# Performance work log

Measured on AMD Instinct MI355X. Metric: run time of the kernel, lower is better.

The kernel has to match this reference:

```python
import jax, jax.numpy as jnp
import numpy as np

TEMPERATURE = 0.1
PROTO_M = 0.999
EPS = 1e-12


def _l2norm(x, axis):
    return x / jnp.clip(jnp.linalg.norm(x, axis=axis, keepdims=True), EPS)


def setup_inputs() -> dict:
    key = jax.random.key(0)
    k1, k2, k3, k4, k5 = jax.random.split(key, 5)
    B, D, K, C = 1024, 128, 65536, 1000
    q = _l2norm(jax.random.normal(k1, (B, D), dtype=jnp.float32), axis=1)
    k = _l2norm(jax.random.normal(k2, (B, D), dtype=jnp.float32), axis=1)
    queue = _l2norm(jax.random.normal(k3, (D, K), dtype=jnp.float32), axis=0)
    prototypes = _l2norm(jax.random.normal(k4, (C, D), dtype=jnp.float32), axis=1)
    target = jax.random.randint(k5, (B,), 0, C, dtype=jnp.int64)
    return {"q": q, "k": k, "queue": queue, "prototypes": prototypes, "target": target}


def reference(q, k, queue, prototypes, target):
    B = q.shape[0]
    C = prototypes.shape[0]

    # contrastive logits: positive is q.k, negatives against the queue
    l_pos = jnp.einsum('nc,nc->n', q, k)[:, None]            # [B, 1]
    l_neg = jnp.einsum('nc,ck->nk', q, queue)                # [B, K]
    logits = jnp.concatenate([l_pos, l_neg], axis=1) / TEMPERATURE

    # prototypical logits
    logits_proto = jnp.einsum('nc,pc->np', q, prototypes) / TEMPERATURE  # [B, C]

    # dequeue/enqueue: ptr = 0 (single device, fresh queue_ptr)
    new_queue = jax.lax.dynamic_update_slice(queue, k.T, (0, 0))

    # sequential per-sample prototype EMA, vectorized in closed form:
    # if class c receives features f_1..f_m (in batch order), the final value is
    #   proto_c * m_p^m + (1 - m_p) * sum_j m_p^(m - j) * f_j
    onehot = jax.nn.one_hot(target, C, dtype=q.dtype)        # [B, C]
    cum = jnp.cumsum(onehot, axis=0)                         # inclusive per-class counts
    occ = jnp.take_along_axis(cum, target[:, None], axis=1)[:, 0]  # j for each sample
    n_c = cum[-1]                                            # [C] total hits per class
    w = (1.0 - PROTO_M) * PROTO_M ** (n_c[target] - occ)     # [B]
    acc = jax.ops.segment_sum(w[:, None] * q, target, num_segments=C)  # [C, D]
    new_prototypes = prototypes * (PROTO_M ** n_c)[:, None] + acc
    new_prototypes = _l2norm(new_prototypes, axis=1)

    return logits, logits_proto, new_queue, new_prototypes
```

## Files before the change

### kernel.cpp

```cpp
#include <hip/hip_runtime.h>
#include <hip/hip_bf16.h>

typedef __bf16 bf16x8 __attribute__((ext_vector_type(8)));
typedef float  f32x4  __attribute__((ext_vector_type(4)));


#define B_   1024
#define D_   128
#define K_   65536
#define C_   1000
#define LROW 65537
#define TINV 10.0f

__global__ __launch_bounds__(256) void prep(const float* __restrict__ queue,
                                            const float* __restrict__ q,
                                            const float* __restrict__ k,
                                            __bf16* __restrict__ Bt,
                                            __bf16* __restrict__ qbf,
                                            float* __restrict__ logits) {
    __shared__ __bf16 Lt[128 * 128];
    const int tid = threadIdx.x;

    if (blockIdx.x < 512) {
        char* ltb = (char*)Lt;
        const int c0 = blockIdx.x * 128;
        #pragma unroll
        for (int it = 0; it < 16; ++it) {
            const int idx = it * 256 + tid;
            const int d   = idx >> 5;
            const int cq  = (idx & 31) * 4;
            const f32x4 v = *reinterpret_cast<const f32x4*>(queue + (size_t)d * K_ + c0 + cq);
            const int db = d >> 3, de = (d & 7) * 2;
            #pragma unroll
            for (int jj = 0; jj < 4; ++jj) {
                const int c = cq + jj;
                *reinterpret_cast<__bf16*>(ltb + c * 256 + ((db ^ ((c >> 2) & 15)) << 4) + de)
                    = (__bf16)v[jj];
            }
        }
        __syncthreads();
        #pragma unroll
        for (int it = 0; it < 8; ++it) {
            const int idx = it * 256 + tid;
            const int c   = idx >> 4;
            const int db  = idx & 15;
            const bf16x8 v = *reinterpret_cast<const bf16x8*>(
                ltb + c * 256 + ((db ^ ((c >> 2) & 15)) << 4));
            *reinterpret_cast<bf16x8*>(Bt + (size_t)(c0 + c) * D_ + db * 8) = v;
        }
    } else {
        const int wid  = tid >> 6;
        const int lane = tid & 63;
        const int row  = (blockIdx.x - 512) * 4 + wid;
        const float2 qv = reinterpret_cast<const float2*>(q + (size_t)row * D_)[lane];
        const float2 kv = reinterpret_cast<const float2*>(k + (size_t)row * D_)[lane];
        union { __bf16 h[2]; unsigned int u; } u2;
        u2.h[0] = (__bf16)(qv.x * TINV);
        u2.h[1] = (__bf16)(qv.y * TINV);
        reinterpret_cast<unsigned int*>(qbf)[row * 64 + lane] = u2.u;
        float p = qv.x * kv.x + qv.y * kv.y;
        #pragma unroll
        for (int off = 32; off > 0; off >>= 1) p += __shfl_xor(p, off);
        if (lane == 0) logits[(size_t)row * LROW] = p * TINV;
    }
}

#define MG_QCOPY 512
#define MG_PROTO 1008
#define MG_PUPD  500
#define MG_PRE   (MG_QCOPY + MG_PROTO + MG_PUPD)
__global__ __launch_bounds__(256) void mega(const __bf16* __restrict__ qbf,
                                            const __bf16* __restrict__ Bt,
                                            const float* __restrict__ queue,
                                            const float* __restrict__ k,
                                            const float* __restrict__ q,
                                            const float* __restrict__ protos,
                                            const int* __restrict__ target,
                                            float* __restrict__ logits,
                                            float* __restrict__ lproto,
                                            float* __restrict__ outq,
                                            float* __restrict__ outp) {
    __shared__ char smem[16384];
    const int tid = threadIdx.x;
    const int bid = blockIdx.x;

    if (bid < MG_QCOPY) {
        const int d  = bid >> 2;
        const int qt = bid & 3;
        const size_t rowoff = (size_t)d * K_;
        const f32x4* src = reinterpret_cast<const f32x4*>(queue + rowoff);
        f32x4*       dst = reinterpret_cast<f32x4*>(outq + rowoff);
        if (qt == 0) {
            #pragma unroll
            for (int i = 0; i < 4; ++i) {
                const int c = i * 256 + tid;
                outq[rowoff + c] = k[(size_t)c * D_ + d];
            }
            #pragma unroll 4
            for (int i = 0; i < 15; ++i) {
                const int idx = 256 + i * 256 + tid;
                dst[idx] = src[idx];
            }
        } else {
            const int base = qt * 4096;
            #pragma unroll 4
            for (int i = 0; i < 16; ++i) {
                const int idx = base + i * 256 + tid;
                dst[idx] = src[idx];
            }
        }

    } else if (bid < MG_QCOPY + MG_PROTO) {
        const int pid  = bid - MG_QCOPY;
        const int bx   = pid % 63, by = pid / 63;
        const int wid  = tid >> 6;
        const int lane = tid & 63;
        const int mrow = (by * 4 + wid) * 16;
        const int ncol = bx * 16;
        const int bl = lane & 15, gk = lane >> 4;
        const int col = ncol + bl;
        const bool valid = (col < C_);

        f32x4 acc = {};
        #pragma unroll
        for (int s = 0; s < 4; ++s) {
            const int koff = s * 32 + gk * 8;
            const float* ap = q + (size_t)(mrow + bl) * D_ + koff;
            bf16x8 a, b;
            #pragma unroll
            for (int v = 0; v < 8; ++v) a[v] = (__bf16)(ap[v] * TINV);
            if (valid) {
                const float* bp = protos + (size_t)col * D_ + koff;
                #pragma unroll
                for (int v = 0; v < 8; ++v) b[v] = (__bf16)bp[v];
            } else {
                #pragma unroll
                for (int v = 0; v < 8; ++v) b[v] = (__bf16)0.0f;
            }
            acc = __builtin_amdgcn_mfma_f32_16x16x32_bf16(a, b, acc, 0, 0, 0);
        }
        #pragma unroll
        for (int r = 0; r < 4; ++r) {
            const int orow = mrow + gk * 4 + r;
            if (valid) lproto[(size_t)orow * C_ + col] = acc[r];
        }

    } else if (bid < MG_PRE) {
        int*   t   = reinterpret_cast<int*>(smem);
        float* red = reinterpret_cast<float*>(smem + 4096);
        const int pid = bid - (MG_QCOPY + MG_PROTO);
        const int sub = tid >> 7;
        const int d   = tid & 127;
        const int c   = pid * 2 + sub;
        for (int i = tid; i < B_; i += 256) t[i] = target[i];
        __syncthreads();

        float acc = 0.0f, wgt = 1.0f;
        int cnt = 0;
        for (int i = 0; i < B_; ++i) {
            if (t[i] == c) {
                ++cnt;
                wgt *= 1.0010010010010010f;
                acc = fmaf(wgt, q[(size_t)i * D_ + d], acc);
            }
        }
        const float val = powf(0.999f, (float)cnt) *
                          fmaf(0.001f, acc, protos[(size_t)c * D_ + d]);

        float ss = val * val;
        #pragma unroll
        for (int off = 32; off > 0; off >>= 1) ss += __shfl_xor(ss, off);
        if ((d & 63) == 0) red[sub * 2 + (d >> 6)] = ss;
        __syncthreads();
        const float norm = sqrtf(red[sub * 2] + red[sub * 2 + 1]);
        outp[(size_t)c * D_ + d] = val / fmaxf(norm, 1e-12f);

    } else {
        __bf16 (*Alds)[128] = reinterpret_cast<__bf16 (*)[128]>(smem);
        const int wid = tid >> 6, lane = tid & 63;
        const int lin = bid - MG_PRE;
        const int xcd = lin & 7, j = lin >> 3;
        const int ctile = xcd * 64 + (j >> 4);
        const int rtile = j & 15;
        const int bcol = ctile * 128;
        const int brow = rtile * 64;

        #pragma unroll
        for (int it = 0; it < 4; ++it) {
            const int idx = it * 256 + tid;
            const int r   = idx >> 4;
            const int cb  = idx & 15;
            const bf16x8 v = *reinterpret_cast<const bf16x8*>(qbf + (size_t)(brow + r) * D_ + cb * 8);
            *reinterpret_cast<bf16x8*>(&Alds[r][(cb ^ (r & 7)) * 8]) = v;
        }
        __syncthreads();

        const int bl = lane & 15, gk = lane >> 4;
        const int colbase = bcol + wid * 32;

        f32x4 acc[4][2] = {};
        #pragma unroll
        for (int s = 0; s < 4; ++s) {
            const int koff = s * 32 + gk * 8;
            bf16x8 af[4];
            #pragma unroll
            for (int m = 0; m < 4; ++m) {
                const int r = m * 16 + bl;
                af[m] = *reinterpret_cast<const bf16x8*>(&Alds[r][((s * 4 + gk) ^ (r & 7)) * 8]);
            }
            #pragma unroll
            for (int n = 0; n < 2; ++n) {
                const bf16x8 bfrag = *reinterpret_cast<const bf16x8*>(
                    Bt + (size_t)(colbase + n * 16 + bl) * D_ + koff);
                #pragma unroll
                for (int m = 0; m < 4; ++m)
                    acc[m][n] = __builtin_amdgcn_mfma_f32_16x16x32_bf16(af[m], bfrag, acc[m][n], 0, 0, 0);
            }
        }

        #pragma unroll
        for (int m = 0; m < 4; ++m)
            #pragma unroll
            for (int n = 0; n < 2; ++n)
                #pragma unroll
                for (int r = 0; r < 4; ++r) {
                    const int orow = brow + m * 16 + (gk << 2) + r;
                    logits[(size_t)orow * LROW + 1 + colbase + n * 16 + bl] = acc[m][n][r];
                }
    }
}

extern "C" void kernel_launch(void* const* d_in, const int* in_sizes, int n_in,
                              void* d_out, int out_size, void* d_ws, size_t ws_size,
                              hipStream_t stream) {
    const float* q      = (const float*)d_in[0];
    const float* k      = (const float*)d_in[1];
    const float* queue  = (const float*)d_in[2];
    const float* protos = (const float*)d_in[3];
    const int*   target = (const int*)d_in[4];

    float* out    = (float*)d_out;
    float* logits = out;
    float* lproto = out + (size_t)B_ * LROW;
    float* outq   = lproto + (size_t)B_ * C_;
    float* outp   = outq + (size_t)D_ * K_;

    __bf16* Bt  = (__bf16*)d_ws;
    __bf16* qbf = (__bf16*)((char*)d_ws + (size_t)K_ * D_ * 2);

    prep<<<512 + 256, 256, 0, stream>>>(queue, q, k, Bt, qbf, logits);
    mega<<<MG_PRE + 8192, 256, 0, stream>>>(qbf, Bt, queue, k, q, protos, target,
                                            logits, lproto, outq, outp);
}
```

Before: 99.24 us.

## Interleave auxiliary work blocks among GEMM blocks in the mega kernel grid

New measurement: 164.3 us. 65.6% more time.

```diff
diff --git a/kernel.cpp b/kernel.cpp
--- a/kernel.cpp
+++ b/kernel.cpp
@@ -81,153 +81,159 @@
                                             float* __restrict__ outq,
                                             float* __restrict__ outp) {
     __shared__ char smem[16384];
-    const int tid = threadIdx.x;
-    const int bid = blockIdx.x;
-
-    if (bid < MG_QCOPY) {
-        const int d  = bid >> 2;
-        const int qt = bid & 3;
-        const size_t rowoff = (size_t)d * K_;
-        const f32x4* src = reinterpret_cast<const f32x4*>(queue + rowoff);
-        f32x4*       dst = reinterpret_cast<f32x4*>(outq + rowoff);
-        if (qt == 0) {
-            #pragma unroll
-            for (int i = 0; i < 4; ++i) {
-                const int c = i * 256 + tid;
-                outq[rowoff + c] = k[(size_t)c * D_ + d];
-            }
-            #pragma unroll 4
-            for (int i = 0; i < 15; ++i) {
-                const int idx = 256 + i * 256 + tid;
-                dst[idx] = src[idx];
-            }
-        } else {
-            const int base = qt * 4096;
-            #pragma unroll 4
-            for (int i = 0; i < 16; ++i) {
-                const int idx = base + i * 256 + tid;
-                dst[idx] = src[idx];
-            }
-        }
-
-    } else if (bid < MG_QCOPY + MG_PROTO) {
-        const int pid  = bid - MG_QCOPY;
-        const int bx   = pid % 63, by = pid / 63;
-        const int wid  = tid >> 6;
-        const int lane = tid & 63;
-        const int mrow = (by * 4 + wid) * 16;
-        const int ncol = bx * 16;
-        const int bl = lane & 15, gk = lane >> 4;
-        const int col = ncol + bl;
-        const bool valid = (col < C_);
-
-        f32x4 acc = {};
-        #pragma unroll
-        for (int s = 0; s < 4; ++s) {
-            const int koff = s * 32 + gk * 8;
-            const float* ap = q + (size_t)(mrow + bl) * D_ + koff;
-            bf16x8 a, b;
-            #pragma unroll
-            for (int v = 0; v < 8; ++v) a[v] = (__bf16)(ap[v] * TINV);
-            if (valid) {
-                const float* bp = protos + (size_t)col * D_ + koff;
+    const int tid  = threadIdx.x;
+    const int bid  = blockIdx.x;
+    const int grp  = bid / 40;
+    const int slot = bid % 40;
+
+    if (slot < 8) {
+        const int pid = ((grp * 8 + slot) * 997) & 2047;
+
+        if (pid < MG_QCOPY) {
+            const int d  = pid >> 2;
+            const int qt = pid & 3;
+            const size_t rowoff = (size_t)d * K_;
+            const f32x4* src = reinterpret_cast<const f32x4*>(queue + rowoff);
+            f32x4*       dst = reinterpret_cast<f32x4*>(outq + rowoff);
+            if (qt == 0) {
                 #pragma unroll
-                for (int v = 0; v < 8; ++v) b[v] = (__bf16)bp[v];
+                for (int i = 0; i < 4; ++i) {
+                    const int c = i * 256 + tid;
+                    outq[rowoff + c] = k[(size_t)c * D_ + d];
+                }
+                #pragma unroll 4
+                for (int i = 0; i < 15; ++i) {
+                    const int idx = 256 + i * 256 + tid;
+                    dst[idx] = src[idx];
+                }
             } else {
+                const int base = qt * 4096;
+                #pragma unroll 4
+                for (int i = 0; i < 16; ++i) {
+                    const int idx = base + i * 256 + tid;
+                    dst[idx] = src[idx];
+                }
+            }
+
+        } else if (pid < MG_QCOPY + MG_PROTO) {
+            const int p2   = pid - MG_QCOPY;
+            const int bx   = p2 % 63, by = p2 / 63;
+            const int wid  = tid >> 6;
+            const int lane = tid & 63;
+            const int mrow = (by * 4 + wid) * 16;
+            const int ncol = bx * 16;
+            const int bl = lane & 15, gk = lane >> 4;
+            const int col = ncol + bl;
+            const bool valid = (col < C_);
+
+            f32x4 acc = {};
+            #pragma unroll
+            for (int s = 0; s < 4; ++s) {
+                const int koff = s * 32 + gk * 8;
+                const float* ap = q + (size_t)(mrow + bl) * D_ + koff;
+                bf16x8 a, b;
                 #pragma unroll
-                for (int v = 0; v < 8; ++v) b[v] = (__bf16)0.0f;
-            }
-            acc = __builtin_amdgcn_mfma_f32_16x16x32_bf16(a, b, acc, 0, 0, 0);
-        }
-        #pragma unroll
-        for (int r = 0; r < 4; ++r) {
-            const int orow = mrow + gk * 4 + r;
-            if (valid) lproto[(size_t)orow * C_ + col] = acc[r];
-        }
-
-    } else if (bid < MG_PRE) {
-        int*   t   = reinterpret_cast<int*>(smem);
-        float* red = reinterpret_cast<float*>(smem + 4096);
-        const int pid = bid - (MG_QCOPY + MG_PROTO);
-        const int sub = tid >> 7;
-        const int d   = tid & 127;
-        const int c   = pid * 2 + sub;
-        for (int i = tid; i < B_; i += 256) t[i] = target[i];
-        __syncthreads();
-
-        float acc = 0.0f, wgt = 1.0f;
-        int cnt = 0;
-        for (int i = 0; i < B_; ++i) {
-            if (t[i] == c) {
-                ++cnt;
-                wgt *= 1.0010010010010010f;
-                acc = fmaf(wgt, q[(size_t)i * D_ + d], acc);
-            }
-        }
-        const float val = powf(0.999f, (float)cnt) *
-                          fmaf(0.001f, acc, protos[(size_t)c * D_ + d]);
-
-        float ss = val * val;
-        #pragma unroll
-        for (int off = 32; off > 0; off >>= 1) ss += __shfl_xor(ss, off);
-        if ((d & 63) == 0) red[sub * 2 + (d >> 6)] = ss;
-        __syncthreads();
-        const float norm = sqrtf(red[sub * 2] + red[sub * 2 + 1]);
-        outp[(size_t)c * D_ + d] = val / fmaxf(norm, 1e-12f);
-
-    } else {
-        __bf16 (*Alds)[128] = reinterpret_cast<__bf16 (*)[128]>(smem);
-        const int wid = tid >> 6, lane = tid & 63;
-        const int lin = bid - MG_PRE;
-        const int xcd = lin & 7, j = lin >> 3;
-        const int ctile = xcd * 64 + (j >> 4);
-        const int rtile = j & 15;
-        const int bcol = ctile * 128;
-        const int brow = rtile * 64;
-
-        #pragma unroll
-        for (int it = 0; it < 4; ++it) {
-            const int idx = it * 256 + tid;
-            const int r   = idx >> 4;
-            const int cb  = idx & 15;
-            const bf16x8 v = *reinterpret_cast<const bf16x8*>(qbf + (size_t)(brow + r) * D_ + cb * 8);
-            *reinterpret_cast<bf16x8*>(&Alds[r][(cb ^ (r & 7)) * 8]) = v;
-        }
-        __syncthreads();
-
-        const int bl = lane & 15, gk = lane >> 4;
-        const int colbase = bcol + wid * 32;
-
-        f32x4 acc[4][2] = {};
-        #pragma unroll
-        for (int s = 0; s < 4; ++s) {
-            const int koff = s * 32 + gk * 8;
-            bf16x8 af[4];
-            #pragma unroll
-            for (int m = 0; m < 4; ++m) {
-                const int r = m * 16 + bl;
-                af[m] = *reinterpret_cast<const bf16x8*>(&Alds[r][((s * 4 + gk) ^ (r & 7)) * 8]);
-            }
-            #pragma unroll
-            for (int n = 0; n < 2; ++n) {
-                const bf16x8 bfrag = *reinterpret_cast<const bf16x8*>(
-                    Bt + (size_t)(colbase + n * 16 + bl) * D_ + koff);
-                #pragma unroll
-                for (int m = 0; m < 4; ++m)
-                    acc[m][n] = __builtin_amdgcn_mfma_f32_16x16x32_bf16(af[m], bfrag, acc[m][n], 0, 0, 0);
-            }
-        }
-
-        #pragma unroll
-        for (int m = 0; m < 4; ++m)
-            #pragma unroll
-            for (int n = 0; n < 2; ++n)
-                #pragma unroll
-                for (int r = 0; r < 4; ++r) {
-                    const int orow = brow + m * 16 + (gk << 2) + r;
-                    logits[(size_t)orow * LROW + 1 + colbase + n * 16 + bl] = acc[m][n][r];
-                }
-    }
+                for (int v = 0; v < 8; ++v) a[v] = (__bf16)(ap[v] * TINV);
+                if (valid) {
+                    const float* bp = protos + (size_t)col * D_ + koff;
+                    #pragma unroll
+                    for (int v = 0; v < 8; ++v) b[v] = (__bf16)bp[v];
+                } else {
+                    #pragma unroll
+                    for (int v = 0; v < 8; ++v) b[v] = (__bf16)0.0f;
+                }
+                acc = __builtin_amdgcn_mfma_f32_16x16x32_bf16(a, b, acc, 0, 0, 0);
+            }
+            #pragma unroll
+            for (int r = 0; r < 4; ++r) {
+                const int orow = mrow + gk * 4 + r;
+                if (valid) lproto[(size_t)orow * C_ + col] = acc[r];
+            }
+
+        } else if (pid < MG_PRE) {
+            int*   t   = reinterpret_cast<int*>(smem);
+            float* red = reinterpret_cast<float*>(smem + 4096);
+            const int p2  = pid - (MG_QCOPY + MG_PROTO);
+            const int sub = tid >> 7;
+            const int d   = tid & 127;
+            const int c   = p2 * 2 + sub;
+            for (int i = tid; i < B_; i += 256) t[i] = target[i];
+            __syncthreads();
+
+            float acc = 0.0f, wgt = 1.0f;
+            int cnt = 0;
+            for (int i = 0; i < B_; ++i) {
+                if (t[i] == c) {
+                    ++cnt;
+                    wgt *= 1.0010010010010010f;
+                    acc = fmaf(wgt, q[(size_t)i * D_ + d], acc);
+                }
+            }
+            const float val = powf(0.999f, (float)cnt) *
+                              fmaf(0.001f, acc, protos[(size_t)c * D_ + d]);
+
+            float ss = val * val;
+            #pragma unroll
+            for (int off = 32; off > 0; off >>= 1) ss += __shfl_xor(ss, off);
+            if ((d & 63) == 0) red[sub * 2 + (d >> 6)] = ss;
+            __syncthreads();
+            const float norm = sqrtf(red[sub * 2] + red[sub * 2 + 1]);
+            outp[(size_t)c * D_ + d] = val / fmaxf(norm, 1e-12f);
+        }
+        return;
+    }
+
+    __bf16 (*Alds)[128] = reinterpret_cast<__bf16 (*)[128]>(smem);
+    const int wid = tid >> 6, lane = tid & 63;
+    const int xcd = slot & 7;
+    const int j   = grp * 4 + ((slot - 8) >> 3);
+    const int ctile = xcd * 64 + (j >> 4);
+    const int rtile = j & 15;
+    const int bcol = ctile * 128;
+    const int brow = rtile * 64;
+
+    #pragma unroll
+    for (int it = 0; it < 4; ++it) {
+        const int idx = it * 256 + tid;
+        const int r   = idx >> 4;
+        const int cb  = idx & 15;
+        const bf16x8 v = *reinterpret_cast<const bf16x8*>(qbf + (size_t)(brow + r) * D_ + cb * 8);
+        *reinterpret_cast<bf16x8*>(&Alds[r][(cb ^ (r & 7)) * 8]) = v;
+    }
+    __syncthreads();
+
+    const int bl = lane & 15, gk = lane >> 4;
+    const int colbase = bcol + wid * 32;
+
+    f32x4 acc[4][2] = {};
+    #pragma unroll
+    for (int s = 0; s < 4; ++s) {
+        const int koff = s * 32 + gk * 8;
+        bf16x8 af[4];
+        #pragma unroll
+        for (int m = 0; m < 4; ++m) {
+            const int r = m * 16 + bl;
+            af[m] = *reinterpret_cast<const bf16x8*>(&Alds[r][((s * 4 + gk) ^ (r & 7)) * 8]);
+        }
+        #pragma unroll
+        for (int n = 0; n < 2; ++n) {
+            const bf16x8 bfrag = *reinterpret_cast<const bf16x8*>(
+                Bt + (size_t)(colbase + n * 16 + bl) * D_ + koff);
+            #pragma unroll
+            for (int m = 0; m < 4; ++m)
+                acc[m][n] = __builtin_amdgcn_mfma_f32_16x16x32_bf16(af[m], bfrag, acc[m][n], 0, 0, 0);
+        }
+    }
+
+    #pragma unroll
+    for (int m = 0; m < 4; ++m)
+        #pragma unroll
+        for (int n = 0; n < 2; ++n)
+            #pragma unroll
+            for (int r = 0; r < 4; ++r) {
+                const int orow = brow + m * 16 + (gk << 2) + r;
+                logits[(size_t)orow * LROW + 1 + colbase + n * 16 + bl] = acc[m][n][r];
+            }
 }
 
 extern "C" void kernel_launch(void* const* d_in, const int* in_sizes, int n_in,
@@ -249,6 +255,6 @@
     __bf16* qbf = (__bf16*)((char*)d_ws + (size_t)K_ * D_ * 2);
 
     prep<<<512 + 256, 256, 0, stream>>>(queue, q, k, Bt, qbf, logits);
-    mega<<<MG_PRE + 8192, 256, 0, stream>>>(qbf, Bt, queue, k, q, protos, target,
-                                            logits, lproto, outq, outp);
+    mega<<<256 * 40, 256, 0, stream>>>(qbf, Bt, queue, k, q, protos, target,
+                                       logits, lproto, outq, outp);
 }
```
